# Kernel tuning notes

Hardware: AMD Instinct MI355X
Metric: run time of the kernel (lower is better)

The kernel has to match this reference:

```python
import jax, jax.numpy as jnp
import numpy as np

B, T, V, D, SLOTS = 16, 4096, 32000, 512, 256
EPS = 1e-5


def setup_inputs() -> dict:
    key = jax.random.key(0)
    ks = jax.random.split(key, 12)
    s = 0.02
    return {
        "seq": jax.random.randint(ks[0], (B, T), 0, V),
        "emb": jax.random.normal(ks[1], (V, D), jnp.float32) * s,
        "w1": jax.random.normal(ks[2], (D, 2 * D), jnp.float32) * s,
        "b1": jnp.zeros((2 * D,), jnp.float32),
        "w2": jax.random.normal(ks[3], (2 * D, D), jnp.float32) * s,
        "b2": jnp.zeros((D,), jnp.float32),
        "ln_g": jnp.ones((D,), jnp.float32),
        "ln_b": jnp.zeros((D,), jnp.float32),
        "wg": jax.random.normal(ks[4], (D,), jnp.float32) * s,
        "bg": jnp.zeros((), jnp.float32),
        "wq": jax.random.normal(ks[5], (D, D), jnp.float32) * s,
        "bq": jnp.zeros((D,), jnp.float32),
        "wo": jax.random.normal(ks[6], (D, V), jnp.float32) * s,
        "bo": jnp.zeros((V,), jnp.float32),
    }


def reference(seq, emb, w1, b1, w2, b2, ln_g, ln_b, wg, bg, wq, bq, wo, bo):
    # Encoder: embed -> residual FFN -> LayerNorm
    h0 = emb[seq]                                        # [B,T,D]
    ff = jax.nn.relu(h0 @ w1 + b1) @ w2 + b2             # [B,T,D]
    x = h0 + ff
    mu = jnp.mean(x, axis=-1, keepdims=True)
    var = jnp.mean(jnp.square(x - mu), axis=-1, keepdims=True)
    h = (x - mu) * jax.lax.rsqrt(var + EPS) * ln_g + ln_b  # [B,T,D]

    # Gate -> top-k slot selection -> gather memory
    gate = jax.nn.sigmoid(h @ wg + bg)                   # [B,T]
    topk = min(SLOTS, T)
    _, top_idx = jax.lax.top_k(gate, topk)               # [B,K]
    memory = jnp.take_along_axis(h, top_idx[:, :, None], axis=1)  # [B,K,D]

    # Single-query masked softmax attention (mask is all ones)
    query_h = h[:, -1, :]                                # [B,D]
    q = query_h @ wq + bq                                # [B,D]
    scores = jnp.einsum('bkd,bd->bk', memory, q)         # [B,K]
    mask = jnp.ones((seq.shape[0], topk), jnp.float32)
    scores = jnp.where(mask == 0, -1e9, scores)
    attn = jax.nn.softmax(scores, axis=-1)               # [B,K]
    ctx = jnp.einsum('bk,bkd->bd', attn, memory)         # [B,D]
    return ctx @ wo + bo                                 # [B,V]
```

## Files before the change

kernel.cpp:

```cpp
#include <hip/hip_runtime.h>

typedef __bf16 bf16x8 __attribute__((ext_vector_type(8)));
typedef float f32x4 __attribute__((ext_vector_type(4)));
typedef unsigned short ushort8v __attribute__((ext_vector_type(8)));

#define NB 16
#define NT 4096
#define NV 32000
#define ND 512
#define NH 1024
#define NSLOTS 256

__device__ __forceinline__ float b2f(unsigned short u) {
  unsigned int x = ((unsigned int)u) << 16;
  return __builtin_bit_cast(float, x);
}
__device__ __forceinline__ unsigned short f2b(float f) {
  unsigned int x = __builtin_bit_cast(unsigned int, f);
  unsigned int r = (x + 0x7FFFu + ((x >> 16) & 1u)) >> 16;
  return (unsigned short)r;
}

#define GLOAD_LDS16(g, l)                                                              \
  __builtin_amdgcn_global_load_lds((const __attribute__((address_space(1))) void*)(g), \
                                   (__attribute__((address_space(3))) void*)(l), 16, 0, 0)

__global__ __launch_bounds__(256) void cvtwt_kernel(
    const float* __restrict__ emb, unsigned short* __restrict__ embb,
    const float* __restrict__ w1, const float* __restrict__ w2,
    unsigned short* __restrict__ w1t, unsigned short* __restrict__ w2t) {
  const int blk = blockIdx.x;
  if (blk < 8000) {
    const long base = ((long)blk * 256 + threadIdx.x) * 8;
    float4 a = *(const float4*)&emb[base];
    float4 b = *(const float4*)&emb[base + 4];
    ushort8v o;
    o[0] = f2b(a.x); o[1] = f2b(a.y); o[2] = f2b(a.z); o[3] = f2b(a.w);
    o[4] = f2b(b.x); o[5] = f2b(b.y); o[6] = f2b(b.z); o[7] = f2b(b.w);
    *(ushort8v*)&embb[base] = o;
  } else {
    const int i = (blk - 8000) * 256 + threadIdx.x;
    if (i < ND * NH) {
      const int n = i >> 9, k = i & 511;
      w1t[i] = f2b(w1[k * NH + n]);
    } else {
      const int j = i - ND * NH;
      const int n = j >> 10, k = j & 1023;
      w2t[j] = f2b(w2[k * ND + n]);
    }
  }
}

template <int KDIM, int NLD, int NBN, bool RELU>
__global__ __launch_bounds__(256) void gemm128_kernel(
    const unsigned short* __restrict__ Abase, const unsigned short* __restrict__ Bt,
    const float* __restrict__ bias, unsigned short* __restrict__ Out) {
  __shared__ union {
    unsigned short AB[3][2][128 * 32];
    unsigned short C[128 * 136];
  } sm;
  const int tid = threadIdx.x;
  const int lane = tid & 63;
  const int w = tid >> 6;

  const int id = blockIdx.x;
  const int swz = (id & 7) * (gridDim.x >> 3) + (id >> 3);
  const int bm = swz / NBN;
  const int bn = swz % NBN;

  const int wm = w >> 1, wn = w & 1;

  const int rgrp = lane >> 2;
  const int schunk = (lane & 3) ^ ((lane >> 3) & 3);
  const unsigned short* aptr[2];
  const unsigned short* bptr[2];
#pragma unroll
  for (int r = 0; r < 2; ++r) {
    const int grp = w * 2 + r;
    const int arow = bm * 128 + grp * 16 + rgrp;
    aptr[r] = Abase + (size_t)arow * (size_t)KDIM + schunk * 8;
    const int brow = bn * 128 + grp * 16 + rgrp;
    bptr[r] = Bt + (size_t)brow * (size_t)KDIM + schunk * 8;
  }

  const int fr = lane & 15;
  const int fhi = lane >> 4;
  const int fsw = (fr >> 1) & 3;
  const int fchunk = (fhi ^ fsw) * 8;
  int aoff[4], boff[4];
#pragma unroll
  for (int m = 0; m < 4; ++m) aoff[m] = (wm * 64 + m * 16 + fr) * 32 + fchunk;
#pragma unroll
  for (int n = 0; n < 4; ++n) boff[n] = (wn * 64 + n * 16 + fr) * 32 + fchunk;

  f32x4 acc[4][4] = {};

  auto stage = [&](int buf, int kt) {
#pragma unroll
    for (int r = 0; r < 2; ++r) {
      const int grp = w * 2 + r;
      GLOAD_LDS16(aptr[r] + kt * 32, &sm.AB[buf][0][grp * 512]);
      GLOAD_LDS16(bptr[r] + kt * 32, &sm.AB[buf][1][grp * 512]);
    }
  };

  constexpr int NKT = KDIM / 32;
  stage(0, 0);
  stage(1, 1);
  for (int kt = 0; kt < NKT; ++kt) {
    if (kt + 1 < NKT)
      asm volatile("s_waitcnt vmcnt(4)" ::: "memory");
    else
      asm volatile("s_waitcnt vmcnt(0)" ::: "memory");
    __builtin_amdgcn_s_barrier();
    if (kt + 2 < NKT) stage((kt + 2) % 3, kt + 2);
    const int cur = kt % 3;
    bf16x8 af[4], bfr[4];
#pragma unroll
    for (int m = 0; m < 4; ++m)
      af[m] = __builtin_bit_cast(bf16x8, *(const ushort8v*)&sm.AB[cur][0][aoff[m]]);
#pragma unroll
    for (int n = 0; n < 4; ++n)
      bfr[n] = __builtin_bit_cast(bf16x8, *(const ushort8v*)&sm.AB[cur][1][boff[n]]);
    __builtin_amdgcn_s_setprio(1);
#pragma unroll
    for (int m = 0; m < 4; ++m)
#pragma unroll
      for (int n = 0; n < 4; ++n)
        acc[m][n] = __builtin_amdgcn_mfma_f32_16x16x32_bf16(af[m], bfr[n], acc[m][n], 0, 0, 0);
    __builtin_amdgcn_s_setprio(0);
  }
  __builtin_amdgcn_s_barrier();

#pragma unroll
  for (int m = 0; m < 4; ++m)
#pragma unroll
    for (int n = 0; n < 4; ++n) {
      const int col_l = wn * 64 + n * 16 + fr;
      const float bb = bias[bn * 128 + col_l];
      const int row_l0 = wm * 64 + m * 16 + (fhi << 2);
#pragma unroll
      for (int i = 0; i < 4; ++i) {
        float v = acc[m][n][i] + bb;
        if constexpr (RELU) v = fmaxf(v, 0.f);
        sm.C[(row_l0 + i) * 136 + col_l] = f2b(v);
      }
    }
  __syncthreads();
#pragma unroll
  for (int r8 = 0; r8 < 8; ++r8) {
    const int chunk = r8 * 256 + tid;
    const int row = chunk >> 4;
    const int c8 = (chunk & 15) * 8;
    ushort8v v = *(const ushort8v*)&sm.C[row * 136 + c8];
    *(ushort8v*)&Out[(size_t)(bm * 128 + row) * (size_t)NLD + bn * 128 + c8] = v;
  }
}

__global__ __launch_bounds__(256) void lnv_kernel(
    const float* __restrict__ emb, const unsigned short* __restrict__ FFv,
    unsigned short* __restrict__ Hv, const float* __restrict__ ln_g,
    const float* __restrict__ ln_b, const float* __restrict__ wg,
    const float* __restrict__ bgp, float* __restrict__ gatev,
    const int* __restrict__ seq, float* __restrict__ hlast) {
  const int lane = threadIdx.x & 63;
  const int w = threadIdx.x >> 6;
  const int v = blockIdx.x * 4 + w;
  const float* er = emb + (size_t)v * ND + lane * 8;
  ushort8v fv = *(const ushort8v*)&FFv[(size_t)v * ND + lane * 8];
  float4 e0 = *(const float4*)er, e1 = *(const float4*)(er + 4);
  float x[8] = {b2f(fv[0]) + e0.x, b2f(fv[1]) + e0.y, b2f(fv[2]) + e0.z, b2f(fv[3]) + e0.w,
                b2f(fv[4]) + e1.x, b2f(fv[5]) + e1.y, b2f(fv[6]) + e1.z, b2f(fv[7]) + e1.w};
  float s = 0.f, sq = 0.f;
#pragma unroll
  for (int j = 0; j < 8; ++j) {
    s += x[j];
    sq += x[j] * x[j];
  }
#pragma unroll
  for (int o = 32; o; o >>= 1) {
    s += __shfl_xor(s, o);
    sq += __shfl_xor(sq, o);
  }
  const float mu = s * (1.f / 512.f);
  const float var = sq * (1.f / 512.f) - mu * mu;
  const float rs = rsqrtf(var + 1e-5f);
  float gd = 0.f;
  float h[8];
  ushort8v hv;
#pragma unroll
  for (int j = 0; j < 8; ++j) {
    const int col = lane * 8 + j;
    h[j] = (x[j] - mu) * rs * ln_g[col] + ln_b[col];
    hv[j] = f2b(h[j]);
    gd += h[j] * wg[col];
  }
  *(ushort8v*)&Hv[(size_t)v * ND + lane * 8] = hv;
#pragma unroll
  for (int o = 32; o; o >>= 1) gd += __shfl_xor(gd, o);
  if (lane == 0) gatev[v] = 1.f / (1.f + expf(-(gd + bgp[0])));
  for (int b = 0; b < NB; ++b) {
    if (seq[b * NT + NT - 1] == v) {
      float* hl = hlast + b * ND + lane * 8;
#pragma unroll
      for (int j = 0; j < 8; ++j) hl[j] = h[j];
    }
  }
}

__global__ __launch_bounds__(256) void topk_qpart_kernel(
    const float* __restrict__ gatev, const int* __restrict__ seq,
    int* __restrict__ topidx, const float* __restrict__ hlast,
    const float* __restrict__ wq, const float* __restrict__ bq,
    float* __restrict__ qpart) {
  __shared__ int wsum[2][4];
  __shared__ unsigned int scanbuf[256];
  const int tid = threadIdx.x;
  if (blockIdx.x >= 16) {
    const int blk = blockIdx.x - 16;
    const int b = blk >> 3, s = blk & 7;
    const int d0 = s * 64;
    float a0 = 0.f, a1 = 0.f;
#pragma unroll 4
    for (int dd = 0; dd < 64; ++dd) {
      const float hv = hlast[b * ND + d0 + dd];
      a0 += hv * wq[(size_t)(d0 + dd) * ND + tid];
      a1 += hv * wq[(size_t)(d0 + dd) * ND + tid + 256];
    }
    if (s == 0) {
      a0 += bq[tid];
      a1 += bq[tid + 256];
    }
    float* qp = qpart + ((size_t)b * 8 + s) * ND;
    qp[tid] = a0;
    qp[tid + 256] = a1;
    return;
  }
  const int b = blockIdx.x;
  const int wv = tid >> 6;
  const int lane = tid & 63;
  const int* sq_ = seq + (size_t)b * NT;
  const int base = tid * 16;
  unsigned int kreg[16];
#pragma unroll
  for (int j = 0; j < 16; ++j)
    kreg[j] = __builtin_bit_cast(unsigned int, gatev[sq_[base + j]]);

  unsigned int K = 0u;
  for (int bit = 29; bit >= 0; --bit) {
    const unsigned int cand = K | (1u << bit);
    int c = 0;
#pragma unroll
    for (int j = 0; j < 16; ++j) c += (kreg[j] >= cand) ? 1 : 0;
#pragma unroll
    for (int o = 32; o; o >>= 1) c += __shfl_xor(c, o);
    const int par = bit & 1;
    if (lane == 0) wsum[par][wv] = c;
    __syncthreads();
    const int tot = wsum[par][0] + wsum[par][1] + wsum[par][2] + wsum[par][3];
    if (tot >= NSLOTS) K = cand;
  }
  int gcnt = 0, ecnt = 0;
#pragma unroll
  for (int j = 0; j < 16; ++j) {
    gcnt += (kreg[j] > K) ? 1 : 0;
    ecnt += (kreg[j] == K) ? 1 : 0;
  }
  __syncthreads();
  scanbuf[tid] = ((unsigned int)gcnt << 16) | (unsigned int)ecnt;
  __syncthreads();
  for (int off = 1; off < 256; off <<= 1) {
    unsigned int v2 = (tid >= off) ? scanbuf[tid - off] : 0u;
    __syncthreads();
    scanbuf[tid] += v2;
    __syncthreads();
  }
  const unsigned int my = scanbuf[tid];
  const unsigned int tot = scanbuf[255];
  const int gi = (int)(my >> 16);
  const int ei = (int)(my & 0xFFFFu);
  const int tot_gt = (int)(tot >> 16);
  int gpos = gi - gcnt;
  int epos = tot_gt + (ei - ecnt);
  int* outp = topidx + b * NSLOTS;
#pragma unroll
  for (int j = 0; j < 16; ++j) {
    if (kreg[j] > K) {
      outp[gpos++] = base + j;
    } else if (kreg[j] == K) {
      if (epos < NSLOTS) outp[epos] = base + j;
      epos++;
    }
  }
}

__global__ __launch_bounds__(256) void attn_kernel(
    const unsigned short* __restrict__ Hv, const int* __restrict__ seq,
    const float* __restrict__ qpart, const int* __restrict__ topidx,
    float* __restrict__ ctx) {
  __shared__ float qs[512];
  __shared__ float attnv[256];
  __shared__ int idxs[256];
  __shared__ float red[4];
  __shared__ float part[2][128];
  const int blk = blockIdx.x;
  const int b = blk >> 2, dc = blk & 3;
  const int tid = threadIdx.x;
  const int lane = tid & 63, wv = tid >> 6;
  {
    float a0 = 0.f, a1 = 0.f;
#pragma unroll
    for (int s = 0; s < 8; ++s) {
      const float* qp = qpart + ((size_t)b * 8 + s) * ND;
      a0 += qp[tid];
      a1 += qp[tid + 256];
    }
    qs[tid] = a0;
    qs[tid + 256] = a1;
  }
  idxs[tid] = seq[(size_t)b * NT + topidx[b * 256 + tid]];
  __syncthreads();
  const unsigned short* hr = Hv + (size_t)idxs[tid] * ND;
  float sc = 0.f;
  for (int d0 = 0; d0 < 512; d0 += 8) {
    ushort8v hv = *(const ushort8v*)&hr[d0];
#pragma unroll
    for (int j = 0; j < 8; ++j) sc += b2f(hv[j]) * qs[d0 + j];
  }
  float m = sc;
#pragma unroll
  for (int o = 32; o; o >>= 1) m = fmaxf(m, __shfl_xor(m, o));
  if (lane == 0) red[wv] = m;
  __syncthreads();
  m = fmaxf(fmaxf(red[0], red[1]), fmaxf(red[2], red[3]));
  __syncthreads();
  const float e = expf(sc - m);
  float ssum = e;
#pragma unroll
  for (int o = 32; o; o >>= 1) ssum += __shfl_xor(ssum, o);
  if (lane == 0) red[wv] = ssum;
  __syncthreads();
  ssum = red[0] + red[1] + red[2] + red[3];
  attnv[tid] = e / ssum;
  __syncthreads();
  const int d = dc * 128 + (tid & 127);
  const int kh = tid >> 7;
  float c = 0.f;
#pragma unroll 4
  for (int k2 = 0; k2 < 128; ++k2) {
    const int k = kh * 128 + k2;
    c += attnv[k] * b2f(Hv[(size_t)idxs[k] * ND + d]);
  }
  part[kh][tid & 127] = c;
  __syncthreads();
  if (tid < 128) ctx[b * 512 + dc * 128 + tid] = part[0][tid] + part[1][tid];
}

__global__ __launch_bounds__(256) void out_fused_kernel(const float* __restrict__ ctx,
                                                        const float* __restrict__ wo,
                                                        const float* __restrict__ bo,
                                                        float* __restrict__ out) {
  __shared__ float cs[16 * 512];
  __shared__ float red[8][16][32];
  const int tid = threadIdx.x;
  const int c = tid & 31, g = tid >> 5;
  const int v0 = blockIdx.x * 32;
  for (int i = tid; i < 16 * 512; i += 256) cs[i] = ctx[i];
  __syncthreads();
  const int d0 = g * 64;
  float acc[16] = {};
  const float* wp = wo + (size_t)d0 * NV + v0 + c;
#pragma unroll 4
  for (int dd = 0; dd < 64; ++dd) {
    const float wv = wp[(size_t)dd * NV];
#pragma unroll
    for (int bb = 0; bb < 16; ++bb) acc[bb] += cs[bb * 512 + d0 + dd] * wv;
  }
#pragma unroll
  for (int bb = 0; bb < 16; ++bb) red[g][bb][c] = acc[bb];
  __syncthreads();
  for (int i = tid; i < 512; i += 256) {
    const int bb = i >> 5, cc = i & 31;
    float a = bo[v0 + cc];
#pragma unroll
    for (int gg = 0; gg < 8; ++gg) a += red[gg][bb][cc];
    out[(size_t)bb * NV + v0 + cc] = a;
  }
}

extern "C" void kernel_launch(void* const* d_in, const int* in_sizes, int n_in,
                              void* d_out, int out_size, void* d_ws, size_t ws_size,
                              hipStream_t stream) {
  const int* seq = (const int*)d_in[0];
  const float* emb = (const float*)d_in[1];
  const float* w1 = (const float*)d_in[2];
  const float* b1 = (const float*)d_in[3];
  const float* w2 = (const float*)d_in[4];
  const float* b2 = (const float*)d_in[5];
  const float* ln_g = (const float*)d_in[6];
  const float* ln_b = (const float*)d_in[7];
  const float* wg = (const float*)d_in[8];
  const float* bg = (const float*)d_in[9];
  const float* wq = (const float*)d_in[10];
  const float* bq = (const float*)d_in[11];
  const float* wo = (const float*)d_in[12];
  const float* bo = (const float*)d_in[13];
  float* out = (float*)d_out;

  char* ws = (char*)d_ws;
  unsigned short* A1v = (unsigned short*)ws;
  unsigned short* FFv = (unsigned short*)(ws + ((size_t)64 << 20));
  unsigned short* embb = (unsigned short*)(ws + ((size_t)96 << 20));
  unsigned short* Hv = (unsigned short*)(ws + ((size_t)128 << 20));
  unsigned short* w1t = (unsigned short*)(ws + ((size_t)177 << 20));
  unsigned short* w2t = (unsigned short*)(ws + ((size_t)178 << 20));
  char* sb = ws + ((size_t)180 << 20);
  float* gatev = (float*)sb;
  int* topidx = (int*)(sb + 131072);
  float* hlast = (float*)(sb + 131072 + 16384);
  float* ctxbuf = (float*)(sb + 131072 + 16384 + 32768);
  float* qpart = (float*)(sb + 131072 + 16384 + 65536);

  cvtwt_kernel<<<12096, 256, 0, stream>>>(emb, embb, w1, w2, w1t, w2t);
  gemm128_kernel<512, 1024, 8, true>
      <<<2000, 256, 0, stream>>>(embb, w1t, b1, A1v);
  gemm128_kernel<1024, 512, 4, false>
      <<<1000, 256, 0, stream>>>(A1v, w2t, b2, FFv);
  lnv_kernel<<<8000, 256, 0, stream>>>(emb, FFv, Hv, ln_g, ln_b, wg, bg, gatev, seq, hlast);
  topk_qpart_kernel<<<144, 256, 0, stream>>>(gatev, seq, topidx, hlast, wq, bq, qpart);
  attn_kernel<<<64, 256, 0, stream>>>(Hv, seq, qpart, topidx, ctxbuf);
  out_fused_kernel<<<1000, 256, 0, stream>>>(ctxbuf, wo, bo, out);
}
```

Before: 199.4 us.

## Fuse second FFN GEMM with LayerNorm and gate into one full-row kernel

```diff
diff --git a/kernel.cpp b/kernel.cpp
--- a/kernel.cpp
+++ b/kernel.cpp
@@ -24,6 +24,8 @@
 #define GLOAD_LDS16(g, l)                                                              \
   __builtin_amdgcn_global_load_lds((const __attribute__((address_space(1))) void*)(g), \
                                    (__attribute__((address_space(3))) void*)(l), 16, 0, 0)
+#define BARRIER() asm volatile("s_barrier" ::: "memory")
+#define VMCNT(n) asm volatile("s_waitcnt vmcnt(" #n ")" ::: "memory")
 
 __global__ __launch_bounds__(256) void cvtwt_kernel(
     const float* __restrict__ emb, unsigned short* __restrict__ embb,
@@ -109,9 +111,9 @@
   stage(1, 1);
   for (int kt = 0; kt < NKT; ++kt) {
     if (kt + 1 < NKT)
-      asm volatile("s_waitcnt vmcnt(4)" ::: "memory");
+      VMCNT(4);
     else
-      asm volatile("s_waitcnt vmcnt(0)" ::: "memory");
+      VMCNT(0);
     __builtin_amdgcn_s_barrier();
     if (kt + 2 < NKT) stage((kt + 2) % 3, kt + 2);
     const int cur = kt % 3;
@@ -157,53 +159,143 @@
   }
 }
 
-__global__ __launch_bounds__(256) void lnv_kernel(
-    const float* __restrict__ emb, const unsigned short* __restrict__ FFv,
-    unsigned short* __restrict__ Hv, const float* __restrict__ ln_g,
-    const float* __restrict__ ln_b, const float* __restrict__ wg,
-    const float* __restrict__ bgp, float* __restrict__ gatev,
+__global__ __launch_bounds__(512, 2) void gemm2ln_kernel(
+    const unsigned short* __restrict__ A1v, const unsigned short* __restrict__ w2t,
+    const float* __restrict__ b2, const float* __restrict__ emb,
+    const float* __restrict__ ln_g, const float* __restrict__ ln_b,
+    const float* __restrict__ wg, const float* __restrict__ bgp,
+    unsigned short* __restrict__ Hv, float* __restrict__ gatev,
     const int* __restrict__ seq, float* __restrict__ hlast) {
-  const int lane = threadIdx.x & 63;
-  const int w = threadIdx.x >> 6;
-  const int v = blockIdx.x * 4 + w;
-  const float* er = emb + (size_t)v * ND + lane * 8;
-  ushort8v fv = *(const ushort8v*)&FFv[(size_t)v * ND + lane * 8];
-  float4 e0 = *(const float4*)er, e1 = *(const float4*)(er + 4);
-  float x[8] = {b2f(fv[0]) + e0.x, b2f(fv[1]) + e0.y, b2f(fv[2]) + e0.z, b2f(fv[3]) + e0.w,
-                b2f(fv[4]) + e1.x, b2f(fv[5]) + e1.y, b2f(fv[6]) + e1.z, b2f(fv[7]) + e1.w};
-  float s = 0.f, sq = 0.f;
-#pragma unroll
-  for (int j = 0; j < 8; ++j) {
-    s += x[j];
-    sq += x[j] * x[j];
-  }
-#pragma unroll
-  for (int o = 32; o; o >>= 1) {
-    s += __shfl_xor(s, o);
-    sq += __shfl_xor(sq, o);
-  }
-  const float mu = s * (1.f / 512.f);
-  const float var = sq * (1.f / 512.f) - mu * mu;
-  const float rs = rsqrtf(var + 1e-5f);
-  float gd = 0.f;
-  float h[8];
-  ushort8v hv;
-#pragma unroll
-  for (int j = 0; j < 8; ++j) {
-    const int col = lane * 8 + j;
-    h[j] = (x[j] - mu) * rs * ln_g[col] + ln_b[col];
-    hv[j] = f2b(h[j]);
-    gd += h[j] * wg[col];
-  }
-  *(ushort8v*)&Hv[(size_t)v * ND + lane * 8] = hv;
-#pragma unroll
-  for (int o = 32; o; o >>= 1) gd += __shfl_xor(gd, o);
-  if (lane == 0) gatev[v] = 1.f / (1.f + expf(-(gd + bgp[0])));
-  for (int b = 0; b < NB; ++b) {
-    if (seq[b * NT + NT - 1] == v) {
-      float* hl = hlast + b * ND + lane * 8;
-#pragma unroll
-      for (int j = 0; j < 8; ++j) hl[j] = h[j];
+  extern __shared__ unsigned short sm2[];
+  const int tid = threadIdx.x;
+  const int lane = tid & 63;
+  const int w = tid >> 6;
+  const int wm = w >> 2;
+  const int wn = w & 3;
+
+  const int id = blockIdx.x, nwg = gridDim.x;
+  const int q = nwg >> 3, r = nwg & 7;
+  const int xcd = id & 7;
+  const int bm = ((xcd < r) ? xcd * (q + 1) : r * (q + 1) + (xcd - r) * q) + (id >> 3);
+
+  const int arow = tid >> 2;
+  const int acol = (tid & 3) ^ ((arow >> 1) & 3);
+  const unsigned short* aptr = A1v + (size_t)(bm * 128 + arow) * NH + acol * 8;
+  const unsigned short* bptr[4];
+#pragma unroll
+  for (int j = 0; j < 4; ++j) {
+    const int c = j * 512 + tid;
+    const int brow = c >> 2;
+    const int bcol = (c & 3) ^ ((brow >> 1) & 3);
+    bptr[j] = w2t + (size_t)brow * NH + bcol * 8;
+  }
+
+  const int fr = lane & 15;
+  const int fhi = lane >> 4;
+  const int fsw = (fr >> 1) & 3;
+  const int fchunk = (fhi ^ fsw) * 8;
+  int aoff[4], boff[8];
+#pragma unroll
+  for (int m = 0; m < 4; ++m) aoff[m] = (wm * 64 + m * 16 + fr) * 32 + fchunk;
+#pragma unroll
+  for (int n = 0; n < 8; ++n) boff[n] = 4096 + (wn * 128 + n * 16 + fr) * 32 + fchunk;
+
+  f32x4 acc[4][8] = {};
+
+  auto stage = [&](int buf, int kt) {
+    unsigned short* base = sm2 + buf * 20480;
+    GLOAD_LDS16(aptr + kt * 32, base + tid * 8);
+#pragma unroll
+    for (int j = 0; j < 4; ++j)
+      GLOAD_LDS16(bptr[j] + kt * 32, base + 4096 + (j * 512 + tid) * 8);
+  };
+
+  constexpr int NKT = NH / 32;
+  stage(0, 0);
+  stage(1, 1);
+  for (int kt = 0; kt < NKT; ++kt) {
+    if (kt + 1 < NKT)
+      VMCNT(5);
+    else
+      VMCNT(0);
+    __builtin_amdgcn_s_barrier();
+    if (kt + 2 < NKT) stage((kt + 2) % 3, kt + 2);
+    const unsigned short* base = sm2 + (kt % 3) * 20480;
+    bf16x8 af[4], bf[8];
+#pragma unroll
+    for (int m = 0; m < 4; ++m)
+      af[m] = __builtin_bit_cast(bf16x8, *(const ushort8v*)&base[aoff[m]]);
+#pragma unroll
+    for (int n = 0; n < 8; ++n)
+      bf[n] = __builtin_bit_cast(bf16x8, *(const ushort8v*)&base[boff[n]]);
+    __builtin_amdgcn_s_setprio(1);
+#pragma unroll
+    for (int m = 0; m < 4; ++m)
+#pragma unroll
+      for (int n = 0; n < 8; ++n)
+        acc[m][n] = __builtin_amdgcn_mfma_f32_16x16x32_bf16(af[m], bf[n], acc[m][n], 0, 0, 0);
+    __builtin_amdgcn_s_setprio(0);
+  }
+  __syncthreads();
+
+  unsigned short* C = sm2;
+  float bb[8];
+#pragma unroll
+  for (int n = 0; n < 8; ++n) bb[n] = b2[wn * 128 + n * 16 + fr];
+#pragma unroll
+  for (int m = 0; m < 4; ++m)
+#pragma unroll
+    for (int n = 0; n < 8; ++n) {
+      const int col_l = wn * 128 + n * 16 + fr;
+      const int row_l0 = wm * 64 + m * 16 + (fhi << 2);
+#pragma unroll
+      for (int i = 0; i < 4; ++i)
+        C[(row_l0 + i) * 516 + col_l] = f2b(acc[m][n][i] + bb[n]);
+    }
+  __syncthreads();
+
+  for (int pass = 0; pass < 16; ++pass) {
+    const int row_l = w + pass * 8;
+    const int vrow = bm * 128 + row_l;
+    ushort8v fv = *(const ushort8v*)&C[row_l * 516 + lane * 8];
+    const float* er = emb + (size_t)vrow * ND + lane * 8;
+    float4 e0 = *(const float4*)er, e1 = *(const float4*)(er + 4);
+    float x[8] = {b2f(fv[0]) + e0.x, b2f(fv[1]) + e0.y, b2f(fv[2]) + e0.z, b2f(fv[3]) + e0.w,
+                  b2f(fv[4]) + e1.x, b2f(fv[5]) + e1.y, b2f(fv[6]) + e1.z, b2f(fv[7]) + e1.w};
+    float s = 0.f, sq = 0.f;
+#pragma unroll
+    for (int j = 0; j < 8; ++j) {
+      s += x[j];
+      sq += x[j] * x[j];
+    }
+#pragma unroll
+    for (int o = 32; o; o >>= 1) {
+      s += __shfl_xor(s, o);
+      sq += __shfl_xor(sq, o);
+    }
+    const float mu = s * (1.f / 512.f);
+    const float var = sq * (1.f / 512.f) - mu * mu;
+    const float rs = rsqrtf(var + 1e-5f);
+    float gd = 0.f;
+    float h[8];
+    ushort8v hv;
+#pragma unroll
+    for (int j = 0; j < 8; ++j) {
+      const int col = lane * 8 + j;
+      h[j] = (x[j] - mu) * rs * ln_g[col] + ln_b[col];
+      hv[j] = f2b(h[j]);
+      gd += h[j] * wg[col];
+    }
+    *(ushort8v*)&Hv[(size_t)vrow * ND + lane * 8] = hv;
+#pragma unroll
+    for (int o = 32; o; o >>= 1) gd += __shfl_xor(gd, o);
+    if (lane == 0) gatev[vrow] = 1.f / (1.f + expf(-(gd + bgp[0])));
+    for (int b = 0; b < NB; ++b) {
+      if (seq[b * NT + NT - 1] == vrow) {
+        float* hl = hlast + b * ND + lane * 8;
+#pragma unroll
+        for (int j = 0; j < 8; ++j) hl[j] = h[j];
+      }
     }
   }
 }
@@ -409,7 +501,6 @@
 
   char* ws = (char*)d_ws;
   unsigned short* A1v = (unsigned short*)ws;
-  unsigned short* FFv = (unsigned short*)(ws + ((size_t)64 << 20));
   unsigned short* embb = (unsigned short*)(ws + ((size_t)96 << 20));
   unsigned short* Hv = (unsigned short*)(ws + ((size_t)128 << 20));
   unsigned short* w1t = (unsigned short*)(ws + ((size_t)177 << 20));
@@ -421,12 +512,14 @@
   float* ctxbuf = (float*)(sb + 131072 + 16384 + 32768);
   float* qpart = (float*)(sb + 131072 + 16384 + 65536);
 
+  hipFuncSetAttribute(reinterpret_cast<const void*>(gemm2ln_kernel),
+                      hipFuncAttributeMaxDynamicSharedMemorySize, 133120);
+
   cvtwt_kernel<<<12096, 256, 0, stream>>>(emb, embb, w1, w2, w1t, w2t);
   gemm128_kernel<512, 1024, 8, true>
       <<<2000, 256, 0, stream>>>(embb, w1t, b1, A1v);
-  gemm128_kernel<1024, 512, 4, false>
-      <<<1000, 256, 0, stream>>>(A1v, w2t, b2, FFv);
-  lnv_kernel<<<8000, 256, 0, stream>>>(emb, FFv, Hv, ln_g, ln_b, wg, bg, gatev, seq, hlast);
+  gemm2ln_kernel<<<250, 512, 133120, stream>>>(A1v, w2t, b2, emb, ln_g, ln_b, wg, bg,
+                                               Hv, gatev, seq, hlast);
   topk_qpart_kernel<<<144, 256, 0, stream>>>(gatev, seq, topidx, hlast, wq, bq, qpart);
   attn_kernel<<<64, 256, 0, stream>>>(Hv, seq, qpart, topidx, ctxbuf);
   out_fused_kernel<<<1000, 256, 0, stream>>>(ctxbuf, wo, bo, out);
```

New measurement: 183.9 us. -7.8%, faster.
